# Kernel tuning notes

Hardware: AMD Instinct MI355X
Metric: run time of the kernel (lower is better)

The kernel has to match this reference:

```python
import jax, jax.numpy as jnp
import numpy as np

N = 100000   # nodes
E = 800000   # directed edges
IN = 256     # in_channels (== hidden, required by repo's vn MLP dims)
HID = 256    # hidden_channels
OUT = 40     # out_channels (arxiv classes)
EPS = 1e-5


def setup_inputs() -> dict:
    key = jax.random.key(0)
    ks = jax.random.split(key, 8)
    def nrm(k, shape, scale=0.05):
        return jax.random.normal(k, shape, dtype=jnp.float32) * scale
    return {
        "x": nrm(ks[0], (N, IN), 1.0),
        "edge_index": jax.random.randint(ks[1], (2, E), 0, N, dtype=jnp.int32),
        # GCNConv weights (PyG: x @ W, then normalized aggregation, then + bias)
        "W0": nrm(ks[2], (IN, HID)),  "b0": jnp.zeros((HID,), jnp.float32),
        "W1": nrm(ks[3], (HID, HID)), "b1": jnp.zeros((HID,), jnp.float32),
        "W2": nrm(ks[4], (HID, OUT)), "b2": jnp.zeros((OUT,), jnp.float32),
        # BatchNorm1d affine params (batch-stat math, training mode)
        "bn_g0": jnp.ones((HID,), jnp.float32), "bn_b0": jnp.zeros((HID,), jnp.float32),
        "bn_g1": jnp.ones((HID,), jnp.float32), "bn_b1": jnp.zeros((HID,), jnp.float32),
        # virtual node embedding (init to 0 per reset_parameters)
        "vn_emb": jnp.zeros((1, IN), jnp.float32),
        # mlp_vns[0]: Linear(IN,HID) + LayerNorm(HID) + ReLU
        "vn_W0": nrm(ks[5], (IN, HID)),  "vn_b0": jnp.zeros((HID,), jnp.float32),
        "ln_g0": jnp.ones((HID,), jnp.float32), "ln_b0": jnp.zeros((HID,), jnp.float32),
        # mlp_vns[1]: Linear(HID,HID) + LayerNorm(HID) + ReLU
        "vn_W1": nrm(ks[6], (HID, HID)), "vn_b1": jnp.zeros((HID,), jnp.float32),
        "ln_g1": jnp.ones((HID,), jnp.float32), "ln_b1": jnp.zeros((HID,), jnp.float32),
    }


def _forward(x, edge_index, W0, b0, W1, b1, W2, b2, bn_g0, bn_b0, bn_g1, bn_b1,
             vn_emb, vn_W0, vn_b0, ln_g0, ln_b0, vn_W1, vn_b1, ln_g1, ln_b1):
    src, dst = edge_index[0], edge_index[1]
    # GCN symmetric normalization with self-loops: deg = in-degree + 1
    deg = jax.ops.segment_sum(jnp.ones(src.shape, jnp.float32), dst, num_segments=N) + 1.0
    dis = jax.lax.rsqrt(deg)                       # deg^{-1/2}  [N]
    coef = (dis[src] * dis[dst])[:, None]          # edge norm   [E,1]
    self_coef = (dis * dis)[:, None]               # self-loop norm = deg^{-1}  [N,1]

    def gcn(h, W, b):
        h = h @ W                                             # [N, out]
        agg = jax.ops.segment_sum(h[src] * coef, dst, num_segments=N)
        return agg + h * self_coef + b

    def bn(h, g, bv):  # BatchNorm1d, batch statistics over nodes
        mu = h.mean(0)
        var = ((h - mu) ** 2).mean(0)
        return (h - mu) * jax.lax.rsqrt(var + EPS) * g + bv

    def ln(h, g, bv):  # LayerNorm over last dim
        mu = h.mean(-1, keepdims=True)
        var = ((h - mu) ** 2).mean(-1, keepdims=True)
        return (h - mu) * jax.lax.rsqrt(var + EPS) * g + bv

    vx = vn_emb                                   # [1, IN]
    # layer 0
    h = x + vx                                    # virtual-node broadcast
    h = gcn(h, W0, b0)
    h = jax.nn.relu(bn(h, bn_g0, bn_b0))          # dropout = identity (eval)
    pool = jnp.sum(h, axis=0, keepdims=True)      # global_add_pool
    vx = jax.nn.relu(ln((pool + vx) @ vn_W0 + vn_b0, ln_g0, ln_b0))
    # layer 1
    h = h + vx
    h = gcn(h, W1, b1)
    h = jax.nn.relu(bn(h, bn_g1, bn_b1))
    pool = jnp.sum(h, axis=0, keepdims=True)
    vx = jax.nn.relu(ln((pool + vx) @ vn_W1 + vn_b1, ln_g1, ln_b1))
    # layer 2 (output)
    h = h + vx
    h = gcn(h, W2, b2)
    return jax.nn.log_softmax(h, axis=-1)


def reference(x, edge_index, W0, b0, W1, b1, W2, b2, bn_g0, bn_b0, bn_g1, bn_b1,
              vn_emb, vn_W0, vn_b0, ln_g0, ln_b0, vn_W1, vn_b1, ln_g1, ln_b1):
    return _forward(x, edge_index, W0, b0, W1, b1, W2, b2, bn_g0, bn_b0, bn_g1, bn_b1,
                    vn_emb, vn_W0, vn_b0, ln_g0, ln_b0, vn_W1, vn_b1, ln_g1, ln_b1)
```

## Files before the change

### kernel.cpp

```cpp
#include <hip/hip_runtime.h>
#include <hip/hip_bf16.h>
#include <cstdint>

#define N_NODES 100000
#define N_EDGES 800000
#define CH      256
#define COUT    40
#define COUTP   48
#define EPS     1e-5f
#define SCAN_CHUNK 1024
#define NSCAN_BLK  98
#define SB_NBLK 500
#define SB_ROWS 200
#define AGG_NPW 16

typedef unsigned short u16;
typedef unsigned int   u32;
typedef short s16x8 __attribute__((ext_vector_type(8)));
typedef float f32x4 __attribute__((ext_vector_type(4)));

__device__ __forceinline__ float b2f(u32 u) { return __uint_as_float(u << 16); }
__device__ __forceinline__ u16 f2b(float f) {
    u32 u = __float_as_uint(f);
    u32 r = (u + 0x7fffu + ((u >> 16) & 1u)) >> 16;
    return (u16)r;
}
__device__ __forceinline__ u32 packb(float a, float b) {
    return (u32)f2b(a) | ((u32)f2b(b) << 16);
}
__device__ __forceinline__ void unpack8(uint4 v, float* f) {
    f[0] = b2f(v.x & 0xffffu); f[1] = b2f(v.x >> 16);
    f[2] = b2f(v.y & 0xffffu); f[3] = b2f(v.y >> 16);
    f[4] = b2f(v.z & 0xffffu); f[5] = b2f(v.z >> 16);
    f[6] = b2f(v.w & 0xffffu); f[7] = b2f(v.w >> 16);
}

__global__ void k_count(const int* __restrict__ dst, int* __restrict__ counts) {
    int e = blockIdx.x * 256 + threadIdx.x;
    if (e < N_EDGES) atomicAdd(&counts[dst[e]], 1);
}

__global__ void k_scan1(const int* __restrict__ counts, int* __restrict__ partial,
                        int* __restrict__ blocksums) {
    __shared__ int sdata[256];
    int base = blockIdx.x * SCAN_CHUNK;
    int t = threadIdx.x;
    int v[4]; int s = 0;
    for (int j = 0; j < 4; j++) {
        int i = base + t * 4 + j;
        v[j] = (i < N_NODES) ? counts[i] : 0;
        s += v[j];
    }
    sdata[t] = s; __syncthreads();
    for (int off = 1; off < 256; off <<= 1) {
        int x = (t >= off) ? sdata[t - off] : 0;
        __syncthreads();
        sdata[t] += x;
        __syncthreads();
    }
    int incl = sdata[t];
    int run = incl - s;
    if (t == 255) blocksums[blockIdx.x] = incl;
    for (int j = 0; j < 4; j++) {
        int i = base + t * 4 + j;
        if (i < N_NODES) partial[i] = run;
        run += v[j];
    }
}

__global__ void k_scan2(int* __restrict__ blocksums) {
    __shared__ int sd[128];
    int t = threadIdx.x;
    int v = (t < NSCAN_BLK) ? blocksums[t] : 0;
    sd[t] = v; __syncthreads();
    for (int off = 1; off < 128; off <<= 1) {
        int x = (t >= off) ? sd[t - off] : 0;
        __syncthreads();
        sd[t] += x;
        __syncthreads();
    }
    if (t < NSCAN_BLK) blocksums[t] = sd[t] - v;
}

__global__ void k_scan3(int* __restrict__ row_start, const int* __restrict__ blocksums,
                        int* __restrict__ cursor, const int* __restrict__ counts,
                        float* __restrict__ dis) {
    int i = blockIdx.x * 256 + threadIdx.x;
    if (i < N_NODES) {
        int v = row_start[i] + blocksums[i >> 10];
        row_start[i] = v;
        cursor[i] = v;
        dis[i] = rsqrtf(1.0f + (float)counts[i]);
    }
}

__global__ void k_fill(const int* __restrict__ src, const int* __restrict__ dst,
                       int* __restrict__ cursor, int* __restrict__ csr,
                       const float* __restrict__ dis, float* __restrict__ coefv) {
    int e = blockIdx.x * 256 + threadIdx.x;
    if (e < N_EDGES) {
        int d = dst[e], s = src[e];
        int p = atomicAdd(&cursor[d], 1);
        csr[p] = s;
        coefv[p] = dis[s] * dis[d];
    }
}

__global__ void k_wt3(const float* __restrict__ W0, const float* __restrict__ W1,
                      const float* __restrict__ W2,
                      u16* __restrict__ T0, u16* __restrict__ T1, u16* __restrict__ T2) {
    int b = blockIdx.x, k = threadIdx.x;
    if (b < 256) {
        T0[b * 256 + k] = f2b(W0[k * 256 + b]);
    } else if (b < 512) {
        int n = b - 256;
        T1[n * 256 + k] = f2b(W1[k * 256 + n]);
    } else {
        int n = b - 512;
        T2[n * 256 + k] = f2b(n < COUT ? W2[k * COUT + n] : 0.f);
    }
}

__global__ void k_xconv(const float* __restrict__ x, u16* __restrict__ xb) {
    int idx = (blockIdx.x * 256 + threadIdx.x) * 8;
    float4 a = *(const float4*)(x + idx);
    float4 b = *(const float4*)(x + idx + 4);
    uint4 o = {packb(a.x, a.y), packb(a.z, a.w), packb(b.x, b.y), packb(b.z, b.w)};
    *(uint4*)(xb + idx) = o;
}

__global__ void k_vecmat(const float* __restrict__ vec, const float* __restrict__ W,
                         int ncols, int npad, float* __restrict__ outv) {
    __shared__ float s[256];
    int t = threadIdx.x;
    s[t] = vec[t];
    __syncthreads();
    float acc = 0.f;
    if (t < ncols) {
        for (int k = 0; k < 256; k++) acc += s[k] * W[k * ncols + t];
    }
    if (t < npad) outv[t] = acc;
}

__global__ __launch_bounds__(256) void k_gemm(const u16* __restrict__ A,
                                              const u16* __restrict__ Wt,
                                              u16* __restrict__ Hout) {
    __shared__ u16 Bs[256 * 72];
    __shared__ u16 As[64 * 72];
    const int t = threadIdx.x;
    const int wave = t >> 6, lane = t & 63;
    const int lm = lane & 15, quad = lane >> 4;
    const int m0 = blockIdx.x * 64;
    const int ar = t >> 2, as_ = (t & 3) * 16;
    const int arow = m0 + ar;
    const f32x4 vz = {0.f, 0.f, 0.f, 0.f};
    f32x4 acc[4][4];
    for (int m = 0; m < 4; m++)
        for (int c = 0; c < 4; c++) acc[m][c] = vz;

    for (int k0 = 0; k0 < 256; k0 += 64) {
        {
            const uint4* bsrc = (const uint4*)(Wt + t * 256 + k0);
            uint4* bdst = (uint4*)(Bs + t * 72);
#pragma unroll
            for (int j = 0; j < 8; j++) bdst[j] = bsrc[j];
            uint4 a0v = {0,0,0,0}, a1v = {0,0,0,0};
            if (arow < N_NODES) {
                const uint4* asrc = (const uint4*)(A + (size_t)arow * 256 + k0 + as_);
                a0v = asrc[0]; a1v = asrc[1];
            }
            uint4* adst = (uint4*)(As + ar * 72 + as_);
            adst[0] = a0v; adst[1] = a1v;
        }
        __syncthreads();
#pragma unroll
        for (int kk = 0; kk < 64; kk += 32) {
            s16x8 af[4], bf[4];
#pragma unroll
            for (int m = 0; m < 4; m++)
                af[m] = *(const s16x8*)(As + (m * 16 + lm) * 72 + kk + quad * 8);
#pragma unroll
            for (int c = 0; c < 4; c++)
                bf[c] = *(const s16x8*)(Bs + (wave * 64 + c * 16 + lm) * 72 + kk + quad * 8);
#pragma unroll
            for (int c = 0; c < 4; c++)
#pragma unroll
                for (int m = 0; m < 4; m++)
                    acc[m][c] = __builtin_amdgcn_mfma_f32_16x16x32_bf16(af[m], bf[c], acc[m][c], 0, 0, 0);
        }
        __syncthreads();
    }
#pragma unroll
    for (int m = 0; m < 4; m++) {
#pragma unroll
        for (int c = 0; c < 4; c++) {
            int col = wave * 64 + c * 16 + lm;
#pragma unroll
            for (int i = 0; i < 4; i++) {
                int row = m0 + m * 16 + quad * 4 + i;
                if (row < N_NODES) Hout[(size_t)row * 256 + col] = f2b(acc[m][c][i]);
            }
        }
    }
}

__global__ __launch_bounds__(256) void k_gemm2(const u16* __restrict__ A,
                                               const u16* __restrict__ Wt,
                                               u16* __restrict__ Hout) {
    __shared__ u16 Bs[48 * 72];
    __shared__ u16 As[64 * 72];
    const int t = threadIdx.x;
    const int wave = t >> 6, lane = t & 63;
    const int lm = lane & 15, quad = lane >> 4;
    const int m0 = blockIdx.x * 64;
    const int ar = t >> 2, as_ = (t & 3) * 16;
    const int arow = m0 + ar;
    const f32x4 vz = {0.f, 0.f, 0.f, 0.f};
    f32x4 acc[3]; acc[0] = vz; acc[1] = vz; acc[2] = vz;

    for (int k0 = 0; k0 < 256; k0 += 64) {
        {
            if (t < 48) {
                const uint4* bsrc = (const uint4*)(Wt + t * 256 + k0);
                uint4* bdst = (uint4*)(Bs + t * 72);
#pragma unroll
                for (int j = 0; j < 8; j++) bdst[j] = bsrc[j];
            }
            uint4 a0v = {0,0,0,0}, a1v = {0,0,0,0};
            if (arow < N_NODES) {
                const uint4* asrc = (const uint4*)(A + (size_t)arow * 256 + k0 + as_);
                a0v = asrc[0]; a1v = asrc[1];
            }
            uint4* adst = (uint4*)(As + ar * 72 + as_);
            adst[0] = a0v; adst[1] = a1v;
        }
        __syncthreads();
#pragma unroll
        for (int kk = 0; kk < 64; kk += 32) {
            s16x8 af = *(const s16x8*)(As + (wave * 16 + lm) * 72 + kk + quad * 8);
#pragma unroll
            for (int c = 0; c < 3; c++) {
                s16x8 bf = *(const s16x8*)(Bs + (c * 16 + lm) * 72 + kk + quad * 8);
                acc[c] = __builtin_amdgcn_mfma_f32_16x16x32_bf16(af, bf, acc[c], 0, 0, 0);
            }
        }
        __syncthreads();
    }
#pragma unroll
    for (int c = 0; c < 3; c++) {
        int col = c * 16 + lm;
#pragma unroll
        for (int i = 0; i < 4; i++) {
            int row = m0 + wave * 16 + quad * 4 + i;
            if (row < N_NODES) Hout[(size_t)row * COUTP + col] = f2b(acc[c][i]);
        }
    }
}

__global__ __launch_bounds__(256) void k_agg(const u16* __restrict__ H2,
                                             const int* __restrict__ row_start,
                                             const int* __restrict__ counts,
                                             const int* __restrict__ csr,
                                             const float* __restrict__ coefv,
                                             const float* __restrict__ dis,
                                             const float* __restrict__ bias,
                                             const float* __restrict__ v2,
                                             u16* __restrict__ OutB,
                                             float* __restrict__ stats) {
    __shared__ float ls[512];
    const int t = threadIdx.x, wave = t >> 6, lane = t & 63, ci = lane * 4;
    const float4 bb = *(const float4*)(bias + ci);
    const float4 vv = *(const float4*)(v2 + ci);
    float s0=0,s1=0,s2=0,s3=0,q0=0,q1=0,q2=0,q3=0;
    const int nbase = blockIdx.x * (4 * AGG_NPW) + wave * AGG_NPW;
    for (int i = 0; i < AGG_NPW; i++) {
        const int node = nbase + i;
        if (node >= N_NODES) break;
        const int beg = row_start[node], cnt = counts[node];
        const float dn = dis[node];
        float a0=0,a1=0,a2=0,a3=0, cs=0;
        int e = 0;
        for (; e + 4 <= cnt; e += 4) {
            int ia = csr[beg+e], ib = csr[beg+e+1], ic = csr[beg+e+2], id = csr[beg+e+3];
            float ca = coefv[beg+e], cb = coefv[beg+e+1], cc = coefv[beg+e+2], cd = coefv[beg+e+3];
            uint2 ra = *(const uint2*)(H2 + (size_t)ia * 256 + ci);
            uint2 rb = *(const uint2*)(H2 + (size_t)ib * 256 + ci);
            uint2 rc = *(const uint2*)(H2 + (size_t)ic * 256 + ci);
            uint2 rd = *(const uint2*)(H2 + (size_t)id * 256 + ci);
            cs += ca + cb + cc + cd;
            a0 += ca*b2f(ra.x&0xffffu) + cb*b2f(rb.x&0xffffu) + cc*b2f(rc.x&0xffffu) + cd*b2f(rd.x&0xffffu);
            a1 += ca*b2f(ra.x>>16)     + cb*b2f(rb.x>>16)     + cc*b2f(rc.x>>16)     + cd*b2f(rd.x>>16);
            a2 += ca*b2f(ra.y&0xffffu) + cb*b2f(rb.y&0xffffu) + cc*b2f(rc.y&0xffffu) + cd*b2f(rd.y&0xffffu);
            a3 += ca*b2f(ra.y>>16)     + cb*b2f(rb.y>>16)     + cc*b2f(rc.y>>16)     + cd*b2f(rd.y>>16);
        }
        for (; e < cnt; e++) {
            int ia = csr[beg+e]; float ca = coefv[beg+e];
            uint2 ra = *(const uint2*)(H2 + (size_t)ia * 256 + ci);
            cs += ca;
            a0 += ca*b2f(ra.x&0xffffu); a1 += ca*b2f(ra.x>>16);
            a2 += ca*b2f(ra.y&0xffffu); a3 += ca*b2f(ra.y>>16);
        }
        uint2 rs = *(const uint2*)(H2 + (size_t)node * 256 + ci);
        const float sc = dn * dn, cv = cs + sc;
        float f0 = a0 + sc*b2f(rs.x&0xffffu) + cv*vv.x + bb.x;
        float f1 = a1 + sc*b2f(rs.x>>16)     + cv*vv.y + bb.y;
        float f2 = a2 + sc*b2f(rs.y&0xffffu) + cv*vv.z + bb.z;
        float f3 = a3 + sc*b2f(rs.y>>16)     + cv*vv.w + bb.w;
        uint2 o; o.x = packb(f0, f1); o.y = packb(f2, f3);
        *(uint2*)(OutB + (size_t)node * 256 + ci) = o;
        s0 += f0; q0 += f0*f0; s1 += f1; q1 += f1*f1;
        s2 += f2; q2 += f2*f2; s3 += f3; q3 += f3*f3;
    }
    ls[t] = 0.f; ls[256 + t] = 0.f;
    __syncthreads();
    atomicAdd(&ls[ci], s0);   atomicAdd(&ls[ci+1], s1);
    atomicAdd(&ls[ci+2], s2); atomicAdd(&ls[ci+3], s3);
    atomicAdd(&ls[256+ci], q0);   atomicAdd(&ls[256+ci+1], q1);
    atomicAdd(&ls[256+ci+2], q2); atomicAdd(&ls[256+ci+3], q3);
    __syncthreads();
    atomicAdd(&stats[t], ls[t]);
    atomicAdd(&stats[256 + t], ls[256 + t]);
}

__global__ __launch_bounds__(256) void k_bnrelu(const u16* __restrict__ OutB,
                                                const float* __restrict__ stats,
                                                const float* __restrict__ g,
                                                const float* __restrict__ bb_,
                                                u16* __restrict__ Hr,
                                                float* __restrict__ pool) {
    __shared__ float lp[256];
    const int t = threadIdx.x;
    const int cg = (t & 31) * 8;
    const int rg = t >> 5;
    const int r0 = blockIdx.x * SB_ROWS + rg;
    const float inv = 1.0f / (float)N_NODES;
    float gg[8], bc[8];
#pragma unroll
    for (int j = 0; j < 8; j++) {
        int c = cg + j;
        float mu = stats[c] * inv;
        float var = stats[256 + c] * inv - mu * mu;
        float rs = rsqrtf(var + EPS);
        gg[j] = g[c] * rs;
        bc[j] = bb_[c] - mu * gg[j];
    }
    float ps[8];
#pragma unroll
    for (int j = 0; j < 8; j++) ps[j] = 0.f;
#pragma unroll 2
    for (int it = 0; it < SB_ROWS / 8; it++) {
        int r = r0 + it * 8;
        uint4 v = *(const uint4*)(OutB + (size_t)r * 256 + cg);
        float f[8]; unpack8(v, f);
#pragma unroll
        for (int j = 0; j < 8; j++) {
            f[j] = fmaxf(f[j] * gg[j] + bc[j], 0.f);
            ps[j] += f[j];
        }
        uint4 o = {packb(f[0], f[1]), packb(f[2], f[3]), packb(f[4], f[5]), packb(f[6], f[7])};
        *(uint4*)(Hr + (size_t)r * 256 + cg) = o;
    }
    lp[t] = 0.f;
    __syncthreads();
#pragma unroll
    for (int j = 0; j < 8; j++) atomicAdd(&lp[cg + j], ps[j]);
    __syncthreads();
    atomicAdd(&pool[t], lp[t]);
}

__global__ void k_vx(const float* __restrict__ pool, const float* __restrict__ vx_old,
                     const float* __restrict__ vnW, const float* __restrict__ vnb,
                     const float* __restrict__ lng, const float* __restrict__ lnb,
                     float* __restrict__ vx_new,
                     const float* __restrict__ Wnext, int ncn, int npn,
                     float* __restrict__ v2n) {
    __shared__ float s[256];
    __shared__ float red[256];
    int t = threadIdx.x;
    s[t] = pool[t] + vx_old[t];
    __syncthreads();
    float y = vnb[t];
    for (int k = 0; k < 256; k++) y += s[k] * vnW[k * 256 + t];
    red[t] = y; __syncthreads();
    for (int off = 128; off > 0; off >>= 1) {
        if (t < off) red[t] += red[t + off];
        __syncthreads();
    }
    float mu = red[0] * (1.f / 256.f);
    __syncthreads();
    float d = y - mu;
    red[t] = d * d; __syncthreads();
    for (int off = 128; off > 0; off >>= 1) {
        if (t < off) red[t] += red[t + off];
        __syncthreads();
    }
    float var = red[0] * (1.f / 256.f);
    float v = fmaxf(d * rsqrtf(var + EPS) * lng[t] + lnb[t], 0.f);
    vx_new[t] = v;
    __syncthreads();
    s[t] = v;
    __syncthreads();
    float acc = 0.f;
    if (t < ncn) {
        for (int k = 0; k < 256; k++) acc += s[k] * Wnext[k * ncn + t];
    }
    if (t < npn) v2n[t] = acc;
}

__global__ __launch_bounds__(256) void k_agg2(const u16* __restrict__ H2,
                                              const int* __restrict__ row_start,
                                              const int* __restrict__ counts,
                                              const int* __restrict__ csr,
                                              const float* __restrict__ coefv,
                                              const float* __restrict__ dis,
                                              const float* __restrict__ bias,
                                              const float* __restrict__ v2,
                                              float* __restrict__ OutF) {
    const int t = threadIdx.x, wave = t >> 6, lane = t & 63;
    const int half = lane >> 5, hl = lane & 31;
    const bool gact = hl < 24;
    const bool cact = hl < 20;
    const int c0 = 2 * hl;
    float bb0 = 0.f, bb1 = 0.f, vv0 = 0.f, vv1 = 0.f;
    if (cact) {
        float2 bv = *(const float2*)(bias + c0); bb0 = bv.x; bb1 = bv.y;
        float2 vvv = *(const float2*)(v2 + c0);  vv0 = vvv.x; vv1 = vvv.y;
    }
    const int nbase = blockIdx.x * 16 + wave * 4;
    for (int i = 0; i < 4; i++) {
        const int node = nbase + i;
        const int beg = row_start[node], cnt = counts[node];
        const float dn = dis[node];
        float a0 = 0.f, a1 = 0.f, cs = 0.f;
        int e = half;
        for (; e + 6 < cnt; e += 8) {
            int ia = csr[beg+e], ib = csr[beg+e+2], ic = csr[beg+e+4], id = csr[beg+e+6];
            float ca = coefv[beg+e], cb = coefv[beg+e+2], cc = coefv[beg+e+4], cd = coefv[beg+e+6];
            u32 ra = 0, rb = 0, rc = 0, rd = 0;
            if (gact) {
                ra = *(const u32*)(H2 + (size_t)ia * COUTP + c0);
                rb = *(const u32*)(H2 + (size_t)ib * COUTP + c0);
                rc = *(const u32*)(H2 + (size_t)ic * COUTP + c0);
                rd = *(const u32*)(H2 + (size_t)id * COUTP + c0);
            }
            cs += ca + cb + cc + cd;
            a0 += ca*b2f(ra&0xffffu) + cb*b2f(rb&0xffffu) + cc*b2f(rc&0xffffu) + cd*b2f(rd&0xffffu);
            a1 += ca*b2f(ra>>16)     + cb*b2f(rb>>16)     + cc*b2f(rc>>16)     + cd*b2f(rd>>16);
        }
        for (; e < cnt; e += 2) {
            int ia = csr[beg+e]; float ca = coefv[beg+e];
            u32 ra = gact ? *(const u32*)(H2 + (size_t)ia * COUTP + c0) : 0u;
            cs += ca;
            a0 += ca*b2f(ra&0xffffu); a1 += ca*b2f(ra>>16);
        }
        a0 += __shfl_xor(a0, 32);
        a1 += __shfl_xor(a1, 32);
        cs += __shfl_xor(cs, 32);
        const float sc = dn * dn;
        u32 rs_ = gact ? *(const u32*)(H2 + (size_t)node * COUTP + c0) : 0u;
        float h0 = a0 + sc*b2f(rs_&0xffffu) + (cs+sc)*vv0 + bb0;
        float h1 = a1 + sc*b2f(rs_>>16)     + (cs+sc)*vv1 + bb1;
        float m = cact ? fmaxf(h0, h1) : -3.0e38f;
#pragma unroll
        for (int off = 16; off > 0; off >>= 1) m = fmaxf(m, __shfl_xor(m, off));
        float ex = cact ? (expf(h0 - m) + expf(h1 - m)) : 0.f;
        float se = ex;
#pragma unroll
        for (int off = 16; off > 0; off >>= 1) se += __shfl_xor(se, off);
        float lg = logf(se);
        if (cact && half == 0) {
            float2 o = {h0 - m - lg, h1 - m - lg};
            *(float2*)(OutF + (size_t)node * COUT + c0) = o;
        }
    }
}

extern "C" void kernel_launch(void* const* d_in, const int* in_sizes, int n_in,
                              void* d_out, int out_size, void* d_ws, size_t ws_size,
                              hipStream_t stream) {
    const float* x   = (const float*)d_in[0];
    const int*   ei  = (const int*)d_in[1];
    const int*   esrc = ei;
    const int*   edst = ei + N_EDGES;
    const float* W0 = (const float*)d_in[2];  const float* b0 = (const float*)d_in[3];
    const float* W1 = (const float*)d_in[4];  const float* b1 = (const float*)d_in[5];
    const float* W2 = (const float*)d_in[6];  const float* b2 = (const float*)d_in[7];
    const float* bg0 = (const float*)d_in[8]; const float* bb0 = (const float*)d_in[9];
    const float* bg1 = (const float*)d_in[10]; const float* bb1 = (const float*)d_in[11];
    const float* vn_emb = (const float*)d_in[12];
    const float* vW0 = (const float*)d_in[13]; const float* vb0 = (const float*)d_in[14];
    const float* lg0 = (const float*)d_in[15]; const float* lb0 = (const float*)d_in[16];
    const float* vW1 = (const float*)d_in[17]; const float* vb1 = (const float*)d_in[18];
    const float* lg1 = (const float*)d_in[19]; const float* lb1 = (const float*)d_in[20];

    char* w = (char*)d_ws;
    auto alloc = [&](size_t bytes) { void* p = (void*)w; w += ((bytes + 255) / 256) * 256; return p; };
    u16* H2    = (u16*)alloc((size_t)N_NODES * 256 * 2);
    u16* HR    = (u16*)alloc((size_t)N_NODES * 256 * 2);
    u16* OutB  = (u16*)alloc((size_t)N_NODES * 256 * 2);
    int* csr   = (int*)alloc((size_t)N_EDGES * 4);
    float* coefv = (float*)alloc((size_t)N_EDGES * 4);
    int* counts = (int*)alloc((size_t)N_NODES * 4);
    int* rowst  = (int*)alloc((size_t)N_NODES * 4);
    int* cursor = (int*)alloc((size_t)N_NODES * 4);
    float* dis  = (float*)alloc((size_t)N_NODES * 4);
    u16* Wtb0 = (u16*)alloc(256 * 256 * 2);
    u16* Wtb1 = (u16*)alloc(256 * 256 * 2);
    u16* Wt2b = (u16*)alloc(COUTP * 256 * 2);
    int* scanblk = (int*)alloc(128 * 4);
    float* stats = (float*)alloc(768 * 4);
    float* vxA = (float*)alloc(256 * 4);
    float* vxB = (float*)alloc(256 * 4);
    float* v20 = (float*)alloc(256 * 4);
    float* v21 = (float*)alloc(256 * 4);
    float* v22 = (float*)alloc(64 * 4);
    (void)ws_size; (void)in_sizes; (void)n_in; (void)out_size; (void)vxB;

    hipMemsetAsync(counts, 0, (size_t)N_NODES * 4, stream);
    k_count<<<(N_EDGES + 255) / 256, 256, 0, stream>>>(edst, counts);
    k_scan1<<<NSCAN_BLK, 256, 0, stream>>>(counts, rowst, scanblk);
    k_scan2<<<1, 128, 0, stream>>>(scanblk);
    k_scan3<<<(N_NODES + 255) / 256, 256, 0, stream>>>(rowst, scanblk, cursor, counts, dis);
    k_fill<<<(N_EDGES + 255) / 256, 256, 0, stream>>>(esrc, edst, cursor, csr, dis, coefv);

    k_wt3<<<512 + COUTP, 256, 0, stream>>>(W0, W1, W2, Wtb0, Wtb1, Wt2b);
    k_xconv<<<(N_NODES * 256 / 8 + 255) / 256, 256, 0, stream>>>(x, HR);
    k_vecmat<<<1, 256, 0, stream>>>(vn_emb, W0, 256, 256, v20);

    const int aggblk = (N_NODES + 63) / 64;

    k_gemm<<<(N_NODES + 63) / 64, 256, 0, stream>>>(HR, Wtb0, H2);
    hipMemsetAsync(stats, 0, 768 * 4, stream);
    k_agg<<<aggblk, 256, 0, stream>>>(H2, rowst, counts, csr, coefv, dis, b0, v20, OutB, stats);
    k_bnrelu<<<SB_NBLK, 256, 0, stream>>>(OutB, stats, bg0, bb0, HR, stats + 512);
    k_vx<<<1, 256, 0, stream>>>(stats + 512, vn_emb, vW0, vb0, lg0, lb0, vxA, W1, 256, 256, v21);

    k_gemm<<<(N_NODES + 63) / 64, 256, 0, stream>>>(HR, Wtb1, H2);
    hipMemsetAsync(stats, 0, 768 * 4, stream);
    k_agg<<<aggblk, 256, 0, stream>>>(H2, rowst, counts, csr, coefv, dis, b1, v21, OutB, stats);
    k_bnrelu<<<SB_NBLK, 256, 0, stream>>>(OutB, stats, bg1, bb1, HR, stats + 512);
    k_vx<<<1, 256, 0, stream>>>(stats + 512, vxA, vW1, vb1, lg1, lb1, vxB, W2, COUT, COUTP, v22);

    k_gemm2<<<(N_NODES + 63) / 64, 256, 0, stream>>>(HR, Wt2b, H2);
    k_agg2<<<N_NODES / 16, 256, 0, stream>>>(H2, rowst, counts, csr, coefv, dis, b2, v22, (float*)d_out);
}
```

Baseline: 785.9 us.

## Fuse fp32-to-bf16 input conversion into first GEMM and widen aggregation loads

Drops the separate x conversion kernel; the first-layer GEMM now reads fp32 rows of x directly and packs them to bf16 while staging into shared memory. This saves one full write and read of a bf16 copy of x. Separately, the aggregation kernel gives each half-wave its own node with 8 channels per lane, using 16-byte gathers instead of 8-byte ones, so two nodes are processed concurrently per wave. The cost is more registers per lane in the aggregation and a GEMM A-load of twice the bytes.

```diff
diff --git a/kernel.cpp b/kernel.cpp
--- a/kernel.cpp
+++ b/kernel.cpp
@@ -12,7 +12,6 @@
 #define NSCAN_BLK  98
 #define SB_NBLK 500
 #define SB_ROWS 200
-#define AGG_NPW 16
 
 typedef unsigned short u16;
 typedef unsigned int   u32;
@@ -119,14 +118,6 @@
         int n = b - 512;
         T2[n * 256 + k] = f2b(n < COUT ? W2[k * COUT + n] : 0.f);
     }
-}
-
-__global__ void k_xconv(const float* __restrict__ x, u16* __restrict__ xb) {
-    int idx = (blockIdx.x * 256 + threadIdx.x) * 8;
-    float4 a = *(const float4*)(x + idx);
-    float4 b = *(const float4*)(x + idx + 4);
-    uint4 o = {packb(a.x, a.y), packb(a.z, a.w), packb(b.x, b.y), packb(b.z, b.w)};
-    *(uint4*)(xb + idx) = o;
 }
 
 __global__ void k_vecmat(const float* __restrict__ vec, const float* __restrict__ W,
@@ -204,6 +195,72 @@
     }
 }
 
+__global__ __launch_bounds__(256) void k_gemm_f32a(const float* __restrict__ A,
+                                                   const u16* __restrict__ Wt,
+                                                   u16* __restrict__ Hout) {
+    __shared__ u16 Bs[256 * 72];
+    __shared__ u16 As[64 * 72];
+    const int t = threadIdx.x;
+    const int wave = t >> 6, lane = t & 63;
+    const int lm = lane & 15, quad = lane >> 4;
+    const int m0 = blockIdx.x * 64;
+    const int ar = t >> 2, as_ = (t & 3) * 16;
+    const int arow = m0 + ar;
+    const f32x4 vz = {0.f, 0.f, 0.f, 0.f};
+    f32x4 acc[4][4];
+    for (int m = 0; m < 4; m++)
+        for (int c = 0; c < 4; c++) acc[m][c] = vz;
+
+    for (int k0 = 0; k0 < 256; k0 += 64) {
+        {
+            const uint4* bsrc = (const uint4*)(Wt + t * 256 + k0);
+            uint4* bdst = (uint4*)(Bs + t * 72);
+#pragma unroll
+            for (int j = 0; j < 8; j++) bdst[j] = bsrc[j];
+            uint4 p0 = {0,0,0,0}, p1 = {0,0,0,0};
+            if (arow < N_NODES) {
+                const float4* asrc = (const float4*)(A + (size_t)arow * 256 + k0 + as_);
+                float4 x0 = asrc[0], x1 = asrc[1], x2 = asrc[2], x3 = asrc[3];
+                p0.x = packb(x0.x, x0.y); p0.y = packb(x0.z, x0.w);
+                p0.z = packb(x1.x, x1.y); p0.w = packb(x1.z, x1.w);
+                p1.x = packb(x2.x, x2.y); p1.y = packb(x2.z, x2.w);
+                p1.z = packb(x3.x, x3.y); p1.w = packb(x3.z, x3.w);
+            }
+            uint4* adst = (uint4*)(As + ar * 72 + as_);
+            adst[0] = p0; adst[1] = p1;
+        }
+        __syncthreads();
+#pragma unroll
+        for (int kk = 0; kk < 64; kk += 32) {
+            s16x8 af[4], bf[4];
+#pragma unroll
+            for (int m = 0; m < 4; m++)
+                af[m] = *(const s16x8*)(As + (m * 16 + lm) * 72 + kk + quad * 8);
+#pragma unroll
+            for (int c = 0; c < 4; c++)
+                bf[c] = *(const s16x8*)(Bs + (wave * 64 + c * 16 + lm) * 72 + kk + quad * 8);
+#pragma unroll
+            for (int c = 0; c < 4; c++)
+#pragma unroll
+                for (int m = 0; m < 4; m++)
+                    acc[m][c] = __builtin_amdgcn_mfma_f32_16x16x32_bf16(af[m], bf[c], acc[m][c], 0, 0, 0);
+        }
+        __syncthreads();
+    }
+#pragma unroll
+    for (int m = 0; m < 4; m++) {
+#pragma unroll
+        for (int c = 0; c < 4; c++) {
+            int col = wave * 64 + c * 16 + lm;
+#pragma unroll
+            for (int i = 0; i < 4; i++) {
+                int row = m0 + m * 16 + quad * 4 + i;
+                if (row < N_NODES) Hout[(size_t)row * 256 + col] = f2b(acc[m][c][i]);
+            }
+        }
+    }
+}
+
 __global__ __launch_bounds__(256) void k_gemm2(const u16* __restrict__ A,
                                                const u16* __restrict__ Wt,
                                                u16* __restrict__ Hout) {
@@ -268,55 +325,73 @@
                                              u16* __restrict__ OutB,
                                              float* __restrict__ stats) {
     __shared__ float ls[512];
-    const int t = threadIdx.x, wave = t >> 6, lane = t & 63, ci = lane * 4;
-    const float4 bb = *(const float4*)(bias + ci);
-    const float4 vv = *(const float4*)(v2 + ci);
-    float s0=0,s1=0,s2=0,s3=0,q0=0,q1=0,q2=0,q3=0;
-    const int nbase = blockIdx.x * (4 * AGG_NPW) + wave * AGG_NPW;
-    for (int i = 0; i < AGG_NPW; i++) {
+    const int t = threadIdx.x, wave = t >> 6, lane = t & 63;
+    const int half = lane >> 5, hl = lane & 31;
+    const int ci = hl * 8;
+    float bb[8], vv[8];
+    {
+        float4 a = *(const float4*)(bias + ci);
+        float4 b = *(const float4*)(bias + ci + 4);
+        float4 c = *(const float4*)(v2 + ci);
+        float4 d = *(const float4*)(v2 + ci + 4);
+        bb[0]=a.x; bb[1]=a.y; bb[2]=a.z; bb[3]=a.w; bb[4]=b.x; bb[5]=b.y; bb[6]=b.z; bb[7]=b.w;
+        vv[0]=c.x; vv[1]=c.y; vv[2]=c.z; vv[3]=c.w; vv[4]=d.x; vv[5]=d.y; vv[6]=d.z; vv[7]=d.w;
+    }
+    float s[8], q[8];
+#pragma unroll
+    for (int j = 0; j < 8; j++) { s[j] = 0.f; q[j] = 0.f; }
+    const int nbase = blockIdx.x * 64 + wave * 16 + half;
+    for (int i = 0; i < 16; i += 2) {
         const int node = nbase + i;
         if (node >= N_NODES) break;
         const int beg = row_start[node], cnt = counts[node];
         const float dn = dis[node];
-        float a0=0,a1=0,a2=0,a3=0, cs=0;
+        float a[8];
+#pragma unroll
+        for (int j = 0; j < 8; j++) a[j] = 0.f;
+        float cs = 0.f;
         int e = 0;
         for (; e + 4 <= cnt; e += 4) {
             int ia = csr[beg+e], ib = csr[beg+e+1], ic = csr[beg+e+2], id = csr[beg+e+3];
             float ca = coefv[beg+e], cb = coefv[beg+e+1], cc = coefv[beg+e+2], cd = coefv[beg+e+3];
-            uint2 ra = *(const uint2*)(H2 + (size_t)ia * 256 + ci);
-            uint2 rb = *(const uint2*)(H2 + (size_t)ib * 256 + ci);
-            uint2 rc = *(const uint2*)(H2 + (size_t)ic * 256 + ci);
-            uint2 rd = *(const uint2*)(H2 + (size_t)id * 256 + ci);
+            uint4 ra = *(const uint4*)(H2 + (size_t)ia * 256 + ci);
+            uint4 rb = *(const uint4*)(H2 + (size_t)ib * 256 + ci);
+            uint4 rc = *(const uint4*)(H2 + (size_t)ic * 256 + ci);
+            uint4 rd = *(const uint4*)(H2 + (size_t)id * 256 + ci);
             cs += ca + cb + cc + cd;
-            a0 += ca*b2f(ra.x&0xffffu) + cb*b2f(rb.x&0xffffu) + cc*b2f(rc.x&0xffffu) + cd*b2f(rd.x&0xffffu);
-            a1 += ca*b2f(ra.x>>16)     + cb*b2f(rb.x>>16)     + cc*b2f(rc.x>>16)     + cd*b2f(rd.x>>16);
-            a2 += ca*b2f(ra.y&0xffffu) + cb*b2f(rb.y&0xffffu) + cc*b2f(rc.y&0xffffu) + cd*b2f(rd.y&0xffffu);
-            a3 += ca*b2f(ra.y>>16)     + cb*b2f(rb.y>>16)     + cc*b2f(rc.y>>16)     + cd*b2f(rd.y>>16);
+            float fa[8], fb[8], fc[8], fd[8];
+            unpack8(ra, fa); unpack8(rb, fb); unpack8(rc, fc); unpack8(rd, fd);
+#pragma unroll
+            for (int j = 0; j < 8; j++)
+                a[j] += ca * fa[j] + cb * fb[j] + cc * fc[j] + cd * fd[j];
         }
         for (; e < cnt; e++) {
             int ia = csr[beg+e]; float ca = coefv[beg+e];
-            uint2 ra = *(const uint2*)(H2 + (size_t)ia * 256 + ci);
+            uint4 ra = *(const uint4*)(H2 + (size_t)ia * 256 + ci);
             cs += ca;
-            a0 += ca*b2f(ra.x&0xffffu); a1 += ca*b2f(ra.x>>16);
-            a2 += ca*b2f(ra.y&0xffffu); a3 += ca*b2f(ra.y>>16);
-        }
-        uint2 rs = *(const uint2*)(H2 + (size_t)node * 256 + ci);
+            float fa[8]; unpack8(ra, fa);
+#pragma unroll
+            for (int j = 0; j < 8; j++) a[j] += ca * fa[j];
+        }
+        uint4 rs = *(const uint4*)(H2 + (size_t)node * 256 + ci);
+        float fs[8]; unpack8(rs, fs);
         const float sc = dn * dn, cv = cs + sc;
-        float f0 = a0 + sc*b2f(rs.x&0xffffu) + cv*vv.x + bb.x;
-        float f1 = a1 + sc*b2f(rs.x>>16)     + cv*vv.y + bb.y;
-        float f2 = a2 + sc*b2f(rs.y&0xffffu) + cv*vv.z + bb.z;
-        float f3 = a3 + sc*b2f(rs.y>>16)     + cv*vv.w + bb.w;
-        uint2 o; o.x = packb(f0, f1); o.y = packb(f2, f3);
-        *(uint2*)(OutB + (size_t)node * 256 + ci) = o;
-        s0 += f0; q0 += f0*f0; s1 += f1; q1 += f1*f1;
-        s2 += f2; q2 += f2*f2; s3 += f3; q3 += f3*f3;
+        float f[8];
+#pragma unroll
+        for (int j = 0; j < 8; j++) {
+            f[j] = a[j] + sc * fs[j] + cv * vv[j] + bb[j];
+            s[j] += f[j]; q[j] += f[j] * f[j];
+        }
+        uint4 o = {packb(f[0], f[1]), packb(f[2], f[3]), packb(f[4], f[5]), packb(f[6], f[7])};
+        *(uint4*)(OutB + (size_t)node * 256 + ci) = o;
     }
     ls[t] = 0.f; ls[256 + t] = 0.f;
     __syncthreads();
-    atomicAdd(&ls[ci], s0);   atomicAdd(&ls[ci+1], s1);
-    atomicAdd(&ls[ci+2], s2); atomicAdd(&ls[ci+3], s3);
-    atomicAdd(&ls[256+ci], q0);   atomicAdd(&ls[256+ci+1], q1);
-    atomicAdd(&ls[256+ci+2], q2); atomicAdd(&ls[256+ci+3], q3);
+#pragma unroll
+    for (int j = 0; j < 8; j++) {
+        atomicAdd(&ls[ci + j], s[j]);
+        atomicAdd(&ls[256 + ci + j], q[j]);
+    }
     __syncthreads();
     atomicAdd(&stats[t], ls[t]);
     atomicAdd(&stats[256 + t], ls[256 + t]);
@@ -524,12 +599,11 @@
     k_fill<<<(N_EDGES + 255) / 256, 256, 0, stream>>>(esrc, edst, cursor, csr, dis, coefv);
 
     k_wt3<<<512 + COUTP, 256, 0, stream>>>(W0, W1, W2, Wtb0, Wtb1, Wt2b);
-    k_xconv<<<(N_NODES * 256 / 8 + 255) / 256, 256, 0, stream>>>(x, HR);
     k_vecmat<<<1, 256, 0, stream>>>(vn_emb, W0, 256, 256, v20);
 
     const int aggblk = (N_NODES + 63) / 64;
 
-    k_gemm<<<(N_NODES + 63) / 64, 256, 0, stream>>>(HR, Wtb0, H2);
+    k_gemm_f32a<<<(N_NODES + 63) / 64, 256, 0, stream>>>(x, Wtb0, H2);
     hipMemsetAsync(stats, 0, 768 * 4, stream);
     k_agg<<<aggblk, 256, 0, stream>>>(H2, rowst, counts, csr, coefv, dis, b0, v20, OutB, stats);
     k_bnrelu<<<SB_NBLK, 256, 0, stream>>>(OutB, stats, bg0, bb0, HR, stats + 512);
```

Result: no change. 779.1 us (-0.9%).
